# Performance work log

Measured on AMD Instinct MI355X. Metric: run time of the kernel, lower is better.

## Reference

```python
import jax, jax.numpy as jnp
import numpy as np

B, N, C, K = 8, 2048, 512, 1


def setup_inputs() -> dict:
    key = jax.random.key(0)
    ks = jax.random.split(key, 10)
    s = 1.0 / np.sqrt(C)
    f32 = jnp.float32
    return {
        "x": jax.random.normal(ks[0], (B, N, C), f32),
        "neighbors": jax.random.randint(ks[1], (N, K), 0, N),
        "Wq": jax.random.normal(ks[2], (C, C), f32) * s,
        "bq": jnp.zeros((C,), f32),
        "Wk": jax.random.normal(ks[3], (C, C), f32) * s,
        "bk": jnp.zeros((C,), f32),
        "Wv": jax.random.normal(ks[4], (C, C), f32) * s,
        "bv": jnp.zeros((C,), f32),
        "rel_bias": jnp.zeros((K, K), f32),  # nn.Parameter(torch.zeros(k,k))
        "Wo": jax.random.normal(ks[5], (C, C), f32) * s,
        "bo": jnp.zeros((C,), f32),
    }


def reference(x, neighbors, Wq, bq, Wk, bk, Wv, bv, rel_bias, Wo, bo):
    # torch Linear: y = x @ W.T + b
    Q = jnp.einsum("bnc,dc->bnd", x, Wq) + bq
    Kt = jnp.einsum("bnc,dc->bnd", x, Wk) + bk
    V = jnp.einsum("bnc,dc->bnd", x, Wv) + bv

    nbr = neighbors[:, 0]  # [N], the single neighbor of each position (k==1)
    Kn = Kt[:, nbr, :]     # [B,N,C] gathered keys
    Vn = V[:, nbr, :]      # [B,N,C] gathered values (V_neighbors viewed as [B,N,k*C])

    # per-position score q_i . k_{nbr_i} + bias scalar
    s = jnp.einsum("bnc,bnc->bn", Q, Kn) + rel_bias[0, 0]

    # dense NxN score matrix, zeros elsewhere (faithful: softmax includes the zeros)
    scores = jnp.zeros((B, N, N), x.dtype).at[:, jnp.arange(N), nbr].set(s)
    probs = jax.nn.softmax(scores / jnp.asarray(np.sqrt(C), x.dtype), axis=-1)

    out = jnp.einsum("bnm,bmc->bnc", probs, Vn)
    return jnp.einsum("bnc,dc->bnd", out, Wo) + bo
```

## Files before the change

### kernel.cpp

```cpp
#include <hip/hip_runtime.h>
#include <hip/hip_bf16.h>
#include <math.h>

namespace {
constexpr int kB = 8;
constexpr int kN = 2048;
constexpr int kC = 512;
constexpr int kR = kB * kN;
constexpr int kNC = 2 * kC;
constexpr float kInvSqrtC = 0.044194173824159216f;

typedef __attribute__((ext_vector_type(8))) short short8;
typedef __attribute__((ext_vector_type(4))) short short4b;
typedef __attribute__((ext_vector_type(4))) float f32x4;
typedef unsigned short ushort;
}

static __device__ __forceinline__ float bf2f(ushort u) {
  union { unsigned int i; float f; } v; v.i = (unsigned int)u << 16; return v.f;
}
static __device__ __forceinline__ ushort f2bf(float f) {
  __hip_bfloat16 h = __float2bfloat16(f);
  union { __hip_bfloat16 h; ushort u; } cv; cv.h = h; return cv.u;
}

#define GLOAD16(G, L) __builtin_amdgcn_global_load_lds( \
    (const __attribute__((address_space(1))) unsigned int*)(G), \
    (__attribute__((address_space(3))) unsigned int*)(L), 16, 0, 0)

__global__ __launch_bounds__(256) void castw_kernel(
    const float* __restrict__ Wq, const float* __restrict__ Wk,
    const float* __restrict__ Wv, const float* __restrict__ Wo,
    ushort* __restrict__ WqT, ushort* __restrict__ WkT,
    ushort* __restrict__ WvT, ushort* __restrict__ Woh,
    const int* __restrict__ nbr, int* __restrict__ cnt,
    int* __restrict__ jlist, int* __restrict__ cnt_c, int* __restrict__ meta) {
  const int z = blockIdx.z;
  const int t = threadIdx.x;
  if (z == 4) {
    if (blockIdx.x || blockIdx.y) return;
    __shared__ int h[kN];
    __shared__ int wsum[256];
#pragma unroll
    for (int i = 0; i < 8; i++) h[t + i * 256] = 0;
    __syncthreads();
#pragma unroll
    for (int i = 0; i < 8; i++) atomicAdd(&h[nbr[t + i * 256]], 1);
    __syncthreads();
#pragma unroll
    for (int i = 0; i < 8; i++) cnt[t + i * 256] = h[t + i * 256];
    const int base = t * 8;
    int lpre[8], lc = 0;
#pragma unroll
    for (int i = 0; i < 8; i++) { lpre[i] = lc; lc += (h[base + i] > 0) ? 1 : 0; }
    wsum[t] = lc;
    __syncthreads();
    for (int off = 1; off < 256; off <<= 1) {
      const int v = (t >= off) ? wsum[t - off] : 0;
      __syncthreads();
      wsum[t] += v;
      __syncthreads();
    }
    const int excl = (t == 0) ? 0 : wsum[t - 1];
    const int total = wsum[255];
#pragma unroll
    for (int i = 0; i < 8; i++) {
      if (h[base + i] > 0) {
        const int p = excl + lpre[i];
        jlist[p] = base + i;
        cnt_c[p] = h[base + i];
      }
    }
    for (int p = total + t; p < kN; p += 256) { jlist[p] = 0; cnt_c[p] = 0; }
    if (t == 0) meta[0] = total;
    return;
  }
  const int d0 = blockIdx.x * 64, c0 = blockIdx.y * 64;
  if (z == 3) {
#pragma unroll
    for (int i = 0; i < 4; i++) {
      const int row = i * 16 + (t >> 4), col4 = (t & 15) * 4;
      const float4 v = *reinterpret_cast<const float4*>(&Wo[(d0 + row) * kC + c0 + col4]);
      short4b o;
      o[0] = (short)f2bf(v.x); o[1] = (short)f2bf(v.y);
      o[2] = (short)f2bf(v.z); o[3] = (short)f2bf(v.w);
      *reinterpret_cast<short4b*>(&Woh[(d0 + row) * kC + c0 + col4]) = o;
    }
    return;
  }
  __shared__ float ld[64][65];
  const float* S = (z == 0) ? Wq : ((z == 1) ? Wk : Wv);
  ushort* T = (z == 0) ? WqT : ((z == 1) ? WkT : WvT);
#pragma unroll
  for (int i = 0; i < 4; i++) {
    const int dl = i * 16 + (t >> 4), cl4 = (t & 15) * 4;
    const float4 v = *reinterpret_cast<const float4*>(&S[(d0 + dl) * kC + c0 + cl4]);
    ld[dl][cl4 + 0] = v.x; ld[dl][cl4 + 1] = v.y;
    ld[dl][cl4 + 2] = v.z; ld[dl][cl4 + 3] = v.w;
  }
  __syncthreads();
#pragma unroll
  for (int i = 0; i < 4; i++) {
    const int cl = i * 16 + (t >> 4), dl4 = (t & 15) * 4;
    short4b o;
#pragma unroll
    for (int q = 0; q < 4; q++) o[q] = (short)f2bf(ld[dl4 + q][cl]);
    *reinterpret_cast<short4b*>(&T[(size_t)(c0 + cl) * kC + d0 + dl4]) = o;
  }
}

__global__ __launch_bounds__(256) void fold_kernel(
    const ushort* __restrict__ WqT, const ushort* __restrict__ WkT,
    const ushort* __restrict__ Woh, const ushort* __restrict__ WvT,
    ushort* __restrict__ Bh,
    const float* __restrict__ bq, const float* __restrict__ bk, const float* __restrict__ bv,
    float* __restrict__ biascat, float* __restrict__ vbq, float* __restrict__ bqbk) {
  const int t = threadIdx.x, lane = t & 63, w = t >> 6;
  const int z = blockIdx.z;
  if (z == 2) {
    const int fid = blockIdx.y * 8 + blockIdx.x;
    const int gw = fid * 4 + w;
    for (int rr = gw; rr < 1536; rr += 256) {
      const ushort* rowp; const float* vec;
      if (rr < 512)       { rowp = &WqT[(size_t)rr * kC];          vec = bk; }
      else if (rr < 1024) { rowp = &WkT[(size_t)(rr - 512) * kC];  vec = bq; }
      else                { rowp = &Woh[(size_t)(rr - 1024) * kC]; vec = bv; }
      const short8 u = *reinterpret_cast<const short8*>(&rowp[lane * 8]);
      const float4 v0 = *reinterpret_cast<const float4*>(&vec[lane * 8]);
      const float4 v1 = *reinterpret_cast<const float4*>(&vec[lane * 8 + 4]);
      float a = bf2f((ushort)u[0]) * v0.x + bf2f((ushort)u[1]) * v0.y +
                bf2f((ushort)u[2]) * v0.z + bf2f((ushort)u[3]) * v0.w +
                bf2f((ushort)u[4]) * v1.x + bf2f((ushort)u[5]) * v1.y +
                bf2f((ushort)u[6]) * v1.z + bf2f((ushort)u[7]) * v1.w;
#pragma unroll
      for (int off = 32; off; off >>= 1) a += __shfl_xor(a, off);
      if (lane == 0) {
        if (rr < 512) biascat[rr] = a;
        else if (rr < 1024) vbq[rr - 512] = a;
        else biascat[rr - 512] = a;
      }
    }
    if (gw == 0) {
      const float4 q0 = *reinterpret_cast<const float4*>(&bq[lane * 8]);
      const float4 q1 = *reinterpret_cast<const float4*>(&bq[lane * 8 + 4]);
      const float4 k0 = *reinterpret_cast<const float4*>(&bk[lane * 8]);
      const float4 k1 = *reinterpret_cast<const float4*>(&bk[lane * 8 + 4]);
      float s = q0.x * k0.x + q0.y * k0.y + q0.z * k0.z + q0.w * k0.w +
                q1.x * k1.x + q1.y * k1.y + q1.z * k1.z + q1.w * k1.w;
#pragma unroll
      for (int off = 32; off; off >>= 1) s += __shfl_xor(s, off);
      if (lane == 0) bqbk[0] = s;
    }
    return;
  }
  __shared__ ushort lA[64 * 64];
  __shared__ ushort lB[64 * 64];
  const ushort* Ap = z ? Woh : WqT;
  const ushort* Bp = z ? WvT : WkT;
  const int r0 = blockIdx.y * 64, c0 = blockIdx.x * 64;
  const int wr = (w >> 1) * 32, wc = (w & 1) * 32;
  const int srow = t >> 3, scol = (t & 7) * 8;
  f32x4 acc[2][2] = {};
  for (int k0 = 0; k0 < kC; k0 += 64) {
#pragma unroll
    for (int it = 0; it < 2; it++) {
      GLOAD16(&Ap[(size_t)(r0 + it * 32 + srow) * kC + k0 + scol], &lA[(it * 32 + srow) * 64 + scol]);
      GLOAD16(&Bp[(size_t)(c0 + it * 32 + srow) * kC + k0 + scol], &lB[(it * 32 + srow) * 64 + scol]);
    }
    __syncthreads();
#pragma unroll
    for (int kk = 0; kk < 2; kk++) {
      const int ko = kk * 32 + (lane >> 4) * 8;
      short8 af[2], bfr[2];
#pragma unroll
      for (int i = 0; i < 2; i++)
        af[i] = *reinterpret_cast<const short8*>(&lA[(wr + i * 16 + (lane & 15)) * 64 + ko]);
#pragma unroll
      for (int j = 0; j < 2; j++)
        bfr[j] = *reinterpret_cast<const short8*>(&lB[(wc + j * 16 + (lane & 15)) * 64 + ko]);
#pragma unroll
      for (int i = 0; i < 2; i++)
#pragma unroll
        for (int j = 0; j < 2; j++)
          acc[i][j] = __builtin_amdgcn_mfma_f32_16x16x32_bf16(af[i], bfr[j], acc[i][j], 0, 0, 0);
    }
    __syncthreads();
  }
#pragma unroll
  for (int j = 0; j < 2; j++) {
    const int col = c0 + wc + j * 16 + (lane & 15);
#pragma unroll
    for (int i = 0; i < 2; i++) {
      const int rbase = r0 + wr + i * 16 + (lane >> 4) * 4;
#pragma unroll
      for (int q = 0; q < 4; q++)
        Bh[(size_t)(z * kC + rbase + q) * kC + col] = f2bf(acc[i][j][q]);
    }
  }
}

__global__ __launch_bounds__(256) void castg_kernel(
    const float* __restrict__ x, const float* __restrict__ vbq,
    ushort* __restrict__ xh, float* __restrict__ g) {
  const int wid = threadIdx.x >> 6, lane = threadIdx.x & 63;
  const int r = blockIdx.x * 4 + wid;
  const float4 a = *reinterpret_cast<const float4*>(&x[(size_t)r * kC + lane * 8]);
  const float4 b = *reinterpret_cast<const float4*>(&x[(size_t)r * kC + lane * 8 + 4]);
  short8 o;
  o[0] = (short)f2bf(a.x); o[1] = (short)f2bf(a.y);
  o[2] = (short)f2bf(a.z); o[3] = (short)f2bf(a.w);
  o[4] = (short)f2bf(b.x); o[5] = (short)f2bf(b.y);
  o[6] = (short)f2bf(b.z); o[7] = (short)f2bf(b.w);
  *reinterpret_cast<short8*>(&xh[(size_t)r * kC + lane * 8]) = o;
  const float4 v0 = *reinterpret_cast<const float4*>(&vbq[lane * 8]);
  const float4 v1 = *reinterpret_cast<const float4*>(&vbq[lane * 8 + 4]);
  float acc = a.x * v0.x + a.y * v0.y + a.z * v0.z + a.w * v0.w +
              b.x * v1.x + b.y * v1.y + b.z * v1.z + b.w * v1.w;
#pragma unroll
  for (int off = 32; off; off >>= 1) acc += __shfl_xor(acc, off);
  if (lane == 0) g[r] = acc;
}

__global__ __launch_bounds__(256) void mm_kernel(
    const ushort* __restrict__ xh, const ushort* __restrict__ Bh,
    const float* __restrict__ biascat,
    const int* __restrict__ cnt_c, const int* __restrict__ jlist, const int* __restrict__ meta,
    ushort* __restrict__ obuf, float* __restrict__ part2) {
  __shared__ ushort lA[2][128 * 64];
  __shared__ ushort lB[2][128 * 64];
  __shared__ float cs[2][128];
  const int id = blockIdx.x;
  const int orig = (id & 7) * 128 + (id >> 3);
  const int rt = orig >> 3;
  const int c0 = (orig & 7) * 128;
  const int b = rt >> 4, lt = rt & 15;
  const int t = threadIdx.x;
  const bool isVo = (c0 >= 512);
  if (lt * 128 >= meta[0]) {
    if (isVo && t < 128)
      part2[(size_t)(b * 16 + lt) * kC + (c0 - 512) + t] = 0.f;
    return;
  }
  const int lane = t & 63, w = t >> 6;
  const int wr = (w >> 1) * 64, wc = (w & 1) * 64;
  const int srow = t >> 3, scol = (t & 7) * 8;
  int jl[4];
#pragma unroll
  for (int it = 0; it < 4; it++) jl[it] = jlist[lt * 128 + it * 32 + srow];
  f32x4 acc[4][4] = {};

  auto stage = [&](int buf, int k0) {
#pragma unroll
    for (int it = 0; it < 4; it++) {
      GLOAD16(&xh[(size_t)(b * kN + jl[it]) * kC + k0 + scol],
              &lA[buf][(it * 32 + srow) * 64 + scol]);
      GLOAD16(&Bh[(size_t)(c0 + it * 32 + srow) * kC + k0 + scol],
              &lB[buf][(it * 32 + srow) * 64 + scol]);
    }
  };

  stage(0, 0);
  __syncthreads();
  int cur = 0;
#pragma unroll
  for (int ts = 0; ts < 8; ++ts) {
    if (ts < 7) stage(cur ^ 1, (ts + 1) * 64);
#pragma unroll
    for (int kk = 0; kk < 2; kk++) {
      const int ko = kk * 32 + (lane >> 4) * 8;
      short8 af[4], bfr[4];
#pragma unroll
      for (int i = 0; i < 4; i++)
        af[i] = *reinterpret_cast<const short8*>(&lA[cur][(wr + i * 16 + (lane & 15)) * 64 + ko]);
#pragma unroll
      for (int j = 0; j < 4; j++)
        bfr[j] = *reinterpret_cast<const short8*>(&lB[cur][(wc + j * 16 + (lane & 15)) * 64 + ko]);
      __builtin_amdgcn_s_setprio(1);
#pragma unroll
      for (int i = 0; i < 4; i++)
#pragma unroll
        for (int j = 0; j < 4; j++)
          acc[i][j] = __builtin_amdgcn_mfma_f32_16x16x32_bf16(af[i], bfr[j], acc[i][j], 0, 0, 0);
      __builtin_amdgcn_s_setprio(0);
    }
    __syncthreads();
    cur ^= 1;
  }

  const int cbase = lt * 128 + wr + ((lane >> 4) << 2);
  float cw[4][4];
  int rj[4][4];
#pragma unroll
  for (int i = 0; i < 4; i++) {
    const int4 j4 = *reinterpret_cast<const int4*>(&jlist[cbase + i * 16]);
    rj[i][0] = j4.x; rj[i][1] = j4.y; rj[i][2] = j4.z; rj[i][3] = j4.w;
  }
  if (isVo) {
#pragma unroll
    for (int i = 0; i < 4; i++) {
      const int4 c4 = *reinterpret_cast<const int4*>(&cnt_c[cbase + i * 16]);
      cw[i][0] = (float)c4.x; cw[i][1] = (float)c4.y;
      cw[i][2] = (float)c4.z; cw[i][3] = (float)c4.w;
    }
  }
  float psum[4] = {0.f, 0.f, 0.f, 0.f};
#pragma unroll
  for (int j = 0; j < 4; j++) {
    const int col = c0 + wc + j * 16 + (lane & 15);
    const float bias = biascat[col];
#pragma unroll
    for (int i = 0; i < 4; i++) {
#pragma unroll
      for (int q = 0; q < 4; q++) {
        const float v = acc[i][j][q] + bias;
        obuf[(size_t)(b * kN + rj[i][q]) * kNC + col] = f2bf(v);
        if (isVo) psum[j] += v * cw[i][q];
      }
    }
  }
  if (isVo) {
#pragma unroll
    for (int j = 0; j < 4; j++) {
      psum[j] += __shfl_xor(psum[j], 16);
      psum[j] += __shfl_xor(psum[j], 32);
    }
    if (lane < 16) {
#pragma unroll
      for (int j = 0; j < 4; j++) cs[w >> 1][wc + j * 16 + lane] = psum[j];
    }
    __syncthreads();
    if (t < 128) {
      part2[(size_t)(b * 16 + lt) * kC + (c0 - 512) + t] = cs[0][t] + cs[1][t];
    }
  }
}

__global__ __launch_bounds__(256) void svo_reduce_kernel(
    const float* __restrict__ part2, float* __restrict__ svo) {
  const int d = blockIdx.x * 256 + threadIdx.x;
  const int b = blockIdx.y;
  float a = 0.f;
#pragma unroll
  for (int rt = 0; rt < 16; rt++) a += part2[(size_t)(b * 16 + rt) * kC + d];
  svo[b * kC + d] = a;
}

__global__ __launch_bounds__(256) void final_kernel(
    const ushort* __restrict__ xh, const ushort* __restrict__ obuf,
    const float* __restrict__ svo, const float* __restrict__ g, const int* __restrict__ nbr,
    const float* __restrict__ bqbk, const float* __restrict__ rb, const float* __restrict__ bo,
    float* __restrict__ out) {
  const int wid = threadIdx.x >> 6, lane = threadIdx.x & 63;
  const int rg = blockIdx.x * 4 + wid;
  const int b = rg >> 11, n = rg & (kN - 1);
  const int j = nbr[n];
  const int j2 = nbr[j];
  const short8 xv = *reinterpret_cast<const short8*>(&xh[(size_t)rg * kC + lane * 8]);
  const short8 wv = *reinterpret_cast<const short8*>(&obuf[(size_t)(b * kN + j) * kNC + lane * 8]);
  float a = 0.f;
#pragma unroll
  for (int q = 0; q < 8; q++) a += bf2f((ushort)xv[q]) * bf2f((ushort)wv[q]);
#pragma unroll
  for (int off = 32; off; off >>= 1) a += __shfl_xor(a, off);
  const float s = a + g[b * kN + j] + bqbk[0] + rb[0];
  const float tt = s * kInvSqrtC;
  const float e = expf(tt);
  const float inv = 1.0f / (e + (float)(kN - 1));
  const float coef = (e - 1.0f) * inv;
  const short8 vv = *reinterpret_cast<const short8*>(&obuf[(size_t)(b * kN + j2) * kNC + kC + lane * 8]);
  const float4 s0 = *reinterpret_cast<const float4*>(&svo[b * kC + lane * 8]);
  const float4 s1 = *reinterpret_cast<const float4*>(&svo[b * kC + lane * 8 + 4]);
  const float4 b0 = *reinterpret_cast<const float4*>(&bo[lane * 8]);
  const float4 b1 = *reinterpret_cast<const float4*>(&bo[lane * 8 + 4]);
  float4 r0, r1;
  r0.x = s0.x * inv + bf2f((ushort)vv[0]) * coef + b0.x;
  r0.y = s0.y * inv + bf2f((ushort)vv[1]) * coef + b0.y;
  r0.z = s0.z * inv + bf2f((ushort)vv[2]) * coef + b0.z;
  r0.w = s0.w * inv + bf2f((ushort)vv[3]) * coef + b0.w;
  r1.x = s1.x * inv + bf2f((ushort)vv[4]) * coef + b1.x;
  r1.y = s1.y * inv + bf2f((ushort)vv[5]) * coef + b1.y;
  r1.z = s1.z * inv + bf2f((ushort)vv[6]) * coef + b1.z;
  r1.w = s1.w * inv + bf2f((ushort)vv[7]) * coef + b1.w;
  *reinterpret_cast<float4*>(&out[(size_t)rg * kC + lane * 8]) = r0;
  *reinterpret_cast<float4*>(&out[(size_t)rg * kC + lane * 8 + 4]) = r1;
}

extern "C" void kernel_launch(void* const* d_in, const int* in_sizes, int n_in,
                              void* d_out, int out_size, void* d_ws, size_t ws_size,
                              hipStream_t stream) {
  const float* x  = (const float*)d_in[0];
  const int* nbr  = (const int*)d_in[1];
  const float* Wq = (const float*)d_in[2];
  const float* bq = (const float*)d_in[3];
  const float* Wk = (const float*)d_in[4];
  const float* bk = (const float*)d_in[5];
  const float* Wv = (const float*)d_in[6];
  const float* bv = (const float*)d_in[7];
  const float* rb = (const float*)d_in[8];
  const float* Wo = (const float*)d_in[9];
  const float* bo = (const float*)d_in[10];
  float* out = (float*)d_out;

  char* ws = (char*)d_ws;
  size_t off = 0;
  auto alloc = [&](size_t bytes) -> void* {
    void* p = ws + off;
    off = (off + bytes + 255) & ~(size_t)255;
    return p;
  };
  ushort* xh    = (ushort*)alloc((size_t)kR * kC * 2);
  ushort* Bh    = (ushort*)alloc((size_t)kNC * kC * 2);
  ushort* obuf  = (ushort*)alloc((size_t)kR * kNC * 2);
  ushort* WqT   = (ushort*)alloc((size_t)kC * kC * 2);
  ushort* WkT   = (ushort*)alloc((size_t)kC * kC * 2);
  ushort* WvT   = (ushort*)alloc((size_t)kC * kC * 2);
  ushort* Woh   = (ushort*)alloc((size_t)kC * kC * 2);
  float* biascat = (float*)alloc(kNC * 4);
  float* vbq    = (float*)alloc(kC * 4);
  float* bqbk   = (float*)alloc(4);
  int*   cnt    = (int*)alloc(kN * 4);
  int*   jlist  = (int*)alloc(kN * 4);
  int*   cnt_c  = (int*)alloc(kN * 4);
  int*   meta   = (int*)alloc(256);
  float* g      = (float*)alloc((size_t)kR * 4);
  float* svo    = (float*)alloc((size_t)kB * kC * 4);
  float* part2  = (float*)alloc((size_t)kB * 16 * kC * 4);
  (void)ws_size; (void)n_in; (void)in_sizes; (void)out_size;

  castw_kernel<<<dim3(8, 8, 5), 256, 0, stream>>>(Wq, Wk, Wv, Wo, WqT, WkT, WvT, Woh,
                                                  nbr, cnt, jlist, cnt_c, meta);
  fold_kernel<<<dim3(8, 8, 3), 256, 0, stream>>>(WqT, WkT, Woh, WvT, Bh, bq, bk, bv, biascat, vbq, bqbk);
  castg_kernel<<<kR / 4, 256, 0, stream>>>(x, vbq, xh, g);
  mm_kernel<<<1024, 256, 0, stream>>>(xh, Bh, biascat, cnt_c, jlist, meta, obuf, part2);
  svo_reduce_kernel<<<dim3(2, kB), 256, 0, stream>>>(part2, svo);
  final_kernel<<<kR / 4, 256, 0, stream>>>(xh, obuf, svo, g, nbr, bqbk, rb, bo, out);
}
```

Measured before the change: 67.99 us.

## Merge bias folding into cast kernel and x-cast into fold kernel

```diff
diff --git a/kernel.cpp b/kernel.cpp
--- a/kernel.cpp
+++ b/kernel.cpp
@@ -33,10 +33,54 @@
     const float* __restrict__ Wv, const float* __restrict__ Wo,
     ushort* __restrict__ WqT, ushort* __restrict__ WkT,
     ushort* __restrict__ WvT, ushort* __restrict__ Woh,
-    const int* __restrict__ nbr, int* __restrict__ cnt,
-    int* __restrict__ jlist, int* __restrict__ cnt_c, int* __restrict__ meta) {
+    const int* __restrict__ nbr,
+    int* __restrict__ jlist, int* __restrict__ cnt_c, int* __restrict__ meta,
+    const float* __restrict__ bq, const float* __restrict__ bk, const float* __restrict__ bv,
+    float* __restrict__ biascat, float* __restrict__ vbq, float* __restrict__ bqbk) {
   const int z = blockIdx.z;
   const int t = threadIdx.x;
+  if (z == 5) {
+    const int gid = blockIdx.y * 8 + blockIdx.x;
+    if (gid < 2) {
+      const int c = gid * 256 + t;
+      float s = 0.f;
+#pragma unroll 8
+      for (int d = 0; d < kC; d++) s += Wq[d * kC + c] * bk[d];
+      biascat[c] = s;
+    } else if (gid < 4) {
+      const int c = (gid - 2) * 256 + t;
+      float s = 0.f;
+#pragma unroll 8
+      for (int d = 0; d < kC; d++) s += Wk[d * kC + c] * bq[d];
+      vbq[c] = s;
+    } else if (gid < 12) {
+      const int w = t >> 6, lane = t & 63;
+      const int dbase = (gid - 4) * 64 + w * 16;
+      const float4 v0 = *reinterpret_cast<const float4*>(&bv[lane * 8]);
+      const float4 v1 = *reinterpret_cast<const float4*>(&bv[lane * 8 + 4]);
+      for (int i = 0; i < 16; i++) {
+        const int d = dbase + i;
+        const float4 a0 = *reinterpret_cast<const float4*>(&Wo[(size_t)d * kC + lane * 8]);
+        const float4 a1 = *reinterpret_cast<const float4*>(&Wo[(size_t)d * kC + lane * 8 + 4]);
+        float s = a0.x * v0.x + a0.y * v0.y + a0.z * v0.z + a0.w * v0.w +
+                  a1.x * v1.x + a1.y * v1.y + a1.z * v1.z + a1.w * v1.w;
+#pragma unroll
+        for (int off = 32; off; off >>= 1) s += __shfl_xor(s, off);
+        if (lane == 0) biascat[kC + d] = s;
+      }
+    } else if (gid == 12 && t < 64) {
+      const float4 q0 = *reinterpret_cast<const float4*>(&bq[t * 8]);
+      const float4 q1 = *reinterpret_cast<const float4*>(&bq[t * 8 + 4]);
+      const float4 k0 = *reinterpret_cast<const float4*>(&bk[t * 8]);
+      const float4 k1 = *reinterpret_cast<const float4*>(&bk[t * 8 + 4]);
+      float s = q0.x * k0.x + q0.y * k0.y + q0.z * k0.z + q0.w * k0.w +
+                q1.x * k1.x + q1.y * k1.y + q1.z * k1.z + q1.w * k1.w;
+#pragma unroll
+      for (int off = 32; off; off >>= 1) s += __shfl_xor(s, off);
+      if (t == 0) bqbk[0] = s;
+    }
+    return;
+  }
   if (z == 4) {
     if (blockIdx.x || blockIdx.y) return;
     __shared__ int h[kN];
@@ -47,8 +91,6 @@
 #pragma unroll
     for (int i = 0; i < 8; i++) atomicAdd(&h[nbr[t + i * 256]], 1);
     __syncthreads();
-#pragma unroll
-    for (int i = 0; i < 8; i++) cnt[t + i * 256] = h[t + i * 256];
     const int base = t * 8;
     int lpre[8], lc = 0;
 #pragma unroll
@@ -109,48 +151,32 @@
   }
 }
 
-__global__ __launch_bounds__(256) void fold_kernel(
+__global__ __launch_bounds__(256) void foldg_kernel(
     const ushort* __restrict__ WqT, const ushort* __restrict__ WkT,
     const ushort* __restrict__ Woh, const ushort* __restrict__ WvT,
     ushort* __restrict__ Bh,
-    const float* __restrict__ bq, const float* __restrict__ bk, const float* __restrict__ bv,
-    float* __restrict__ biascat, float* __restrict__ vbq, float* __restrict__ bqbk) {
+    const float* __restrict__ x, const float* __restrict__ vbq,
+    ushort* __restrict__ xh, float* __restrict__ g) {
   const int t = threadIdx.x, lane = t & 63, w = t >> 6;
   const int z = blockIdx.z;
-  if (z == 2) {
-    const int fid = blockIdx.y * 8 + blockIdx.x;
-    const int gw = fid * 4 + w;
-    for (int rr = gw; rr < 1536; rr += 256) {
-      const ushort* rowp; const float* vec;
-      if (rr < 512)       { rowp = &WqT[(size_t)rr * kC];          vec = bk; }
-      else if (rr < 1024) { rowp = &WkT[(size_t)(rr - 512) * kC];  vec = bq; }
-      else                { rowp = &Woh[(size_t)(rr - 1024) * kC]; vec = bv; }
-      const short8 u = *reinterpret_cast<const short8*>(&rowp[lane * 8]);
-      const float4 v0 = *reinterpret_cast<const float4*>(&vec[lane * 8]);
-      const float4 v1 = *reinterpret_cast<const float4*>(&vec[lane * 8 + 4]);
-      float a = bf2f((ushort)u[0]) * v0.x + bf2f((ushort)u[1]) * v0.y +
-                bf2f((ushort)u[2]) * v0.z + bf2f((ushort)u[3]) * v0.w +
-                bf2f((ushort)u[4]) * v1.x + bf2f((ushort)u[5]) * v1.y +
-                bf2f((ushort)u[6]) * v1.z + bf2f((ushort)u[7]) * v1.w;
-#pragma unroll
-      for (int off = 32; off; off >>= 1) a += __shfl_xor(a, off);
-      if (lane == 0) {
-        if (rr < 512) biascat[rr] = a;
-        else if (rr < 1024) vbq[rr - 512] = a;
-        else biascat[rr - 512] = a;
-      }
-    }
-    if (gw == 0) {
-      const float4 q0 = *reinterpret_cast<const float4*>(&bq[lane * 8]);
-      const float4 q1 = *reinterpret_cast<const float4*>(&bq[lane * 8 + 4]);
-      const float4 k0 = *reinterpret_cast<const float4*>(&bk[lane * 8]);
-      const float4 k1 = *reinterpret_cast<const float4*>(&bk[lane * 8 + 4]);
-      float s = q0.x * k0.x + q0.y * k0.y + q0.z * k0.z + q0.w * k0.w +
-                q1.x * k1.x + q1.y * k1.y + q1.z * k1.z + q1.w * k1.w;
-#pragma unroll
-      for (int off = 32; off; off >>= 1) s += __shfl_xor(s, off);
-      if (lane == 0) bqbk[0] = s;
-    }
+  if (z >= 2) {
+    const int unit = (z - 2) * 64 + blockIdx.y * 8 + blockIdx.x;
+    const int r = unit * 4 + w;
+    const float4 a = *reinterpret_cast<const float4*>(&x[(size_t)r * kC + lane * 8]);
+    const float4 b = *reinterpret_cast<const float4*>(&x[(size_t)r * kC + lane * 8 + 4]);
+    short8 o;
+    o[0] = (short)f2bf(a.x); o[1] = (short)f2bf(a.y);
+    o[2] = (short)f2bf(a.z); o[3] = (short)f2bf(a.w);
+    o[4] = (short)f2bf(b.x); o[5] = (short)f2bf(b.y);
+    o[6] = (short)f2bf(b.z); o[7] = (short)f2bf(b.w);
+    *reinterpret_cast<short8*>(&xh[(size_t)r * kC + lane * 8]) = o;
+    const float4 v0 = *reinterpret_cast<const float4*>(&vbq[lane * 8]);
+    const float4 v1 = *reinterpret_cast<const float4*>(&vbq[lane * 8 + 4]);
+    float acc = a.x * v0.x + a.y * v0.y + a.z * v0.z + a.w * v0.w +
+                b.x * v1.x + b.y * v1.y + b.z * v1.z + b.w * v1.w;
+#pragma unroll
+    for (int off = 32; off; off >>= 1) acc += __shfl_xor(acc, off);
+    if (lane == 0) g[r] = acc;
     return;
   }
   __shared__ ushort lA[64 * 64];
@@ -197,28 +223,6 @@
         Bh[(size_t)(z * kC + rbase + q) * kC + col] = f2bf(acc[i][j][q]);
     }
   }
-}
-
-__global__ __launch_bounds__(256) void castg_kernel(
-    const float* __restrict__ x, const float* __restrict__ vbq,
-    ushort* __restrict__ xh, float* __restrict__ g) {
-  const int wid = threadIdx.x >> 6, lane = threadIdx.x & 63;
-  const int r = blockIdx.x * 4 + wid;
-  const float4 a = *reinterpret_cast<const float4*>(&x[(size_t)r * kC + lane * 8]);
-  const float4 b = *reinterpret_cast<const float4*>(&x[(size_t)r * kC + lane * 8 + 4]);
-  short8 o;
-  o[0] = (short)f2bf(a.x); o[1] = (short)f2bf(a.y);
-  o[2] = (short)f2bf(a.z); o[3] = (short)f2bf(a.w);
-  o[4] = (short)f2bf(b.x); o[5] = (short)f2bf(b.y);
-  o[6] = (short)f2bf(b.z); o[7] = (short)f2bf(b.w);
-  *reinterpret_cast<short8*>(&xh[(size_t)r * kC + lane * 8]) = o;
-  const float4 v0 = *reinterpret_cast<const float4*>(&vbq[lane * 8]);
-  const float4 v1 = *reinterpret_cast<const float4*>(&vbq[lane * 8 + 4]);
-  float acc = a.x * v0.x + a.y * v0.y + a.z * v0.z + a.w * v0.w +
-              b.x * v1.x + b.y * v1.y + b.z * v1.z + b.w * v1.w;
-#pragma unroll
-  for (int off = 32; off; off >>= 1) acc += __shfl_xor(acc, off);
-  if (lane == 0) g[r] = acc;
 }
 
 __global__ __launch_bounds__(256) void mm_kernel(
@@ -418,7 +422,6 @@
   float* biascat = (float*)alloc(kNC * 4);
   float* vbq    = (float*)alloc(kC * 4);
   float* bqbk   = (float*)alloc(4);
-  int*   cnt    = (int*)alloc(kN * 4);
   int*   jlist  = (int*)alloc(kN * 4);
   int*   cnt_c  = (int*)alloc(kN * 4);
   int*   meta   = (int*)alloc(256);
@@ -427,10 +430,10 @@
   float* part2  = (float*)alloc((size_t)kB * 16 * kC * 4);
   (void)ws_size; (void)n_in; (void)in_sizes; (void)out_size;
 
-  castw_kernel<<<dim3(8, 8, 5), 256, 0, stream>>>(Wq, Wk, Wv, Wo, WqT, WkT, WvT, Woh,
-                                                  nbr, cnt, jlist, cnt_c, meta);
-  fold_kernel<<<dim3(8, 8, 3), 256, 0, stream>>>(WqT, WkT, Woh, WvT, Bh, bq, bk, bv, biascat, vbq, bqbk);
-  castg_kernel<<<kR / 4, 256, 0, stream>>>(x, vbq, xh, g);
+  castw_kernel<<<dim3(8, 8, 6), 256, 0, stream>>>(Wq, Wk, Wv, Wo, WqT, WkT, WvT, Woh,
+                                                  nbr, jlist, cnt_c, meta,
+                                                  bq, bk, bv, biascat, vbq, bqbk);
+  foldg_kernel<<<dim3(8, 8, 66), 256, 0, stream>>>(WqT, WkT, Woh, WvT, Bh, x, vbq, xh, g);
   mm_kernel<<<1024, 256, 0, stream>>>(xh, Bh, biascat, cnt_c, jlist, meta, obuf, part2);
   svo_reduce_kernel<<<dim3(2, kB), 256, 0, stream>>>(part2, svo);
   final_kernel<<<kR / 4, 256, 0, stream>>>(xh, obuf, svo, g, nbr, bqbk, rb, bo, out);
```

Result: slower. 83.58 us (+22.9%).
